# Optimization experiments

Hardware: AMD Instinct MI355X
Metric: run time of the kernel (lower is better)

The kernel has to match this reference:

```python
import jax, jax.numpy as jnp
import numpy as np
import math

B, SQ, SK, HID, NH = 2, 2048, 512, 1024, 16
HD = HID // NH  # head dim = 64


def setup_inputs() -> dict:
    key = jax.random.key(0)
    k1, k2, k3, k4, k5 = jax.random.split(key, 5)
    return {
        "hidden_states": jax.random.normal(k1, (B, SQ, HID), dtype=jnp.float32),
        "encoder_hidden_states": jax.random.normal(k2, (B, SK, HID), dtype=jnp.float32),
        "encoder_attention_mask": jnp.ones((B, SK), dtype=jnp.int32),
        "Wq": jax.random.normal(k3, (HID, HID), dtype=jnp.float32) * (1.0 / math.sqrt(HID)),
        "Wk": jax.random.normal(k4, (HID, HID), dtype=jnp.float32) * (1.0 / math.sqrt(HID)),
        "Wv": jax.random.normal(k5, (HID, HID), dtype=jnp.float32) * (1.0 / math.sqrt(HID)),
    }


def reference(hidden_states, encoder_hidden_states, encoder_attention_mask, Wq, Wk, Wv):
    # nn.Linear(bias=False): y = x @ W.T ; split heads -> [B, H, S, D]
    def split_heads(x, S):
        return x.reshape(x.shape[0], S, NH, HD).transpose(0, 2, 1, 3)

    q = split_heads(hidden_states @ Wq.T, SQ)            # [B,H,Sq,D]
    k = split_heads(encoder_hidden_states @ Wk.T, SK)    # [B,H,Sk,D]
    v = split_heads(encoder_hidden_states @ Wv.T, SK)    # [B,H,Sk,D]

    scores = jnp.einsum("bhqd,bhkd->bhqk", q, k) / math.sqrt(HD)  # [B,H,Sq,Sk]

    # HF-style extended mask: (1 - mask) * finfo.min, broadcast over heads/queries
    neg = jnp.finfo(scores.dtype).min
    inv_mask = (1.0 - encoder_attention_mask.astype(scores.dtype))[:, None, None, :] * neg

    probs = jax.nn.softmax(scores + inv_mask, axis=-1)
    context = jnp.einsum("bhqk,bhkd->bhqd", probs, v)    # [B,H,Sq,D]
    context = context.transpose(0, 2, 1, 3).reshape(hidden_states.shape[0], SQ, HID)
    # NOTE: returned attention_scores are scaled but UNMASKED, matching the source
    return (context, scores)
```

## Files before the change

kernel.cpp:

```cpp
#include <hip/hip_runtime.h>

#define B_   2
#define SQ_  2048
#define SK_  512
#define HID_ 1024
#define NH_  16
#define HD_  64

typedef __bf16 bf16x8 __attribute__((ext_vector_type(8)));
typedef float  f32x4  __attribute__((ext_vector_type(4)));

__device__ __forceinline__ unsigned short f2bf(float f) {
    unsigned u = __builtin_bit_cast(unsigned, f);
    u += 0x7fffu + ((u >> 16) & 1u);
    return (unsigned short)(u >> 16);
}

__device__ __forceinline__ void gll16(const unsigned short* g, unsigned short* l) {
    __builtin_amdgcn_global_load_lds(
        (const __attribute__((address_space(1))) unsigned int*)(const void*)g,
        (__attribute__((address_space(3))) unsigned int*)(void*)l,
        16, 0, 0);
}

__global__ __launch_bounds__(256) void cvt_all(const float* __restrict__ hs,
                                               const float* __restrict__ enc,
                                               const float* __restrict__ wq,
                                               const float* __restrict__ wk,
                                               const float* __restrict__ wv,
                                               unsigned short* __restrict__ hb,
                                               unsigned short* __restrict__ eb,
                                               unsigned short* __restrict__ wqb,
                                               unsigned short* __restrict__ wkb,
                                               unsigned short* __restrict__ wvb) {
    size_t i = ((size_t)blockIdx.x * 256 + threadIdx.x) * 4;
    const float* s; unsigned short* d; size_t off;
    if (i < 4194304)      { s = hs;  d = hb;  off = i; }
    else if (i < 5242880) { s = enc; d = eb;  off = i - 4194304; }
    else if (i < 6291456) { s = wq;  d = wqb; off = i - 5242880; }
    else if (i < 7340032) { s = wk;  d = wkb; off = i - 6291456; }
    else                  { s = wv;  d = wvb; off = i - 7340032; }
    float4 v = *reinterpret_cast<const float4*>(s + off);
    ushort4 o;
    o.x = f2bf(v.x); o.y = f2bf(v.y); o.z = f2bf(v.z); o.w = f2bf(v.w);
    *reinterpret_cast<ushort4*>(d + off) = o;
}

__global__ __launch_bounds__(256, 3) void gemm_qkv(const unsigned short* __restrict__ hb,
                                                   const unsigned short* __restrict__ eb,
                                                   const unsigned short* __restrict__ wq,
                                                   const unsigned short* __restrict__ wk,
                                                   const unsigned short* __restrict__ wv,
                                                   unsigned short* __restrict__ qo,
                                                   unsigned short* __restrict__ ko,
                                                   unsigned short* __restrict__ vo) {
    __shared__ unsigned short as[2][64 * 64];
    __shared__ unsigned short bs[2][128 * 64];

    int bid = blockIdx.x;
    bid = (bid & 7) * 96 + (bid >> 3);
    int nb = bid & 7, ms = bid >> 3;
    const unsigned short* Ab; const unsigned short* Wb;
    int mrow, mode;
    if (ms < 64)      { mode = 0; Ab = hb; Wb = wq; mrow = ms * 64; }
    else if (ms < 80) { mode = 1; Ab = eb; Wb = wk; mrow = (ms - 64) * 64; }
    else              { mode = 2; Ab = eb; Wb = wv; mrow = (ms - 80) * 64; }
    int n0 = nb * 128;

    int tid = threadIdx.x, lane = tid & 63, w = tid >> 6;
    int quad = lane >> 4, lc = lane & 15;

    int lr  = lane >> 3;
    int chg = (lane & 7) ^ lr;

    f32x4 zero4 = {0.f, 0.f, 0.f, 0.f};
    f32x4 acc[4][2];
#pragma unroll
    for (int i = 0; i < 4; i++) { acc[i][0] = zero4; acc[i][1] = zero4; }

    int rsw = lc & 7;

#pragma unroll
    for (int j = 0; j < 2; j++) {
        int c = w * 2 + j;
        gll16(Ab + (size_t)(mrow + c * 8 + lr) * 1024 + chg * 8, &as[0][(c * 8) * 64]);
    }
#pragma unroll
    for (int j = 0; j < 4; j++) {
        int c = w * 4 + j;
        gll16(Wb + (size_t)(n0 + c * 8 + lr) * 1024 + chg * 8, &bs[0][(c * 8) * 64]);
    }
    __syncthreads();

#pragma unroll 2
    for (int it = 0; it < 16; ++it) {
        int cur = it & 1;
        if (it < 15) {
            int k0n = (it + 1) * 64;
#pragma unroll
            for (int j = 0; j < 2; j++) {
                int c = w * 2 + j;
                gll16(Ab + (size_t)(mrow + c * 8 + lr) * 1024 + k0n + chg * 8,
                      &as[cur ^ 1][(c * 8) * 64]);
            }
#pragma unroll
            for (int j = 0; j < 4; j++) {
                int c = w * 4 + j;
                gll16(Wb + (size_t)(n0 + c * 8 + lr) * 1024 + k0n + chg * 8,
                      &bs[cur ^ 1][(c * 8) * 64]);
            }
        }
#pragma unroll
        for (int kk = 0; kk < 2; kk++) {
            bf16x8 af[4], bfr[2];
#pragma unroll
            for (int mt = 0; mt < 4; mt++)
                af[mt] = *reinterpret_cast<const bf16x8*>(
                    &as[cur][(mt * 16 + lc) * 64 + ((kk * 4 + quad) ^ rsw) * 8]);
#pragma unroll
            for (int nt = 0; nt < 2; nt++)
                bfr[nt] = *reinterpret_cast<const bf16x8*>(
                    &bs[cur][(w * 32 + nt * 16 + lc) * 64 + ((kk * 4 + quad) ^ rsw) * 8]);
#pragma unroll
            for (int mt = 0; mt < 4; mt++)
#pragma unroll
                for (int nt = 0; nt < 2; nt++)
                    acc[mt][nt] = __builtin_amdgcn_mfma_f32_16x16x32_bf16(af[mt], bfr[nt], acc[mt][nt], 0, 0, 0);
        }
        __syncthreads();
    }

#pragma unroll
    for (int mt = 0; mt < 4; mt++) {
#pragma unroll
        for (int nt = 0; nt < 2; nt++) {
            int n = n0 + w * 32 + nt * 16 + lc;
            int h = n >> 6, d = n & 63;
#pragma unroll
            for (int r = 0; r < 4; r++) {
                int M = mrow + mt * 16 + quad * 4 + r;
                unsigned short val = f2bf(acc[mt][nt][r]);
                if (mode == 0) {
                    int b = M >> 11, s = M & 2047;
                    qo[(((size_t)(b * NH_ + h)) * SQ_ + s) * HD_ + d] = val;
                } else if (mode == 1) {
                    int b = M >> 9, s = M & 511;
                    ko[(((size_t)(b * NH_ + h)) * SK_ + s) * HD_ + d] = val;
                } else {
                    int b = M >> 9, s = M & 511;
                    vo[(((size_t)(b * NH_ + h)) * HD_ + d) * SK_ + s] = val;
                }
            }
        }
    }
}

#define PST 72

__global__ __launch_bounds__(256, 4) void attn_kernel(const unsigned short* __restrict__ qh,
                                                      const unsigned short* __restrict__ kh,
                                                      const unsigned short* __restrict__ vh,
                                                      const int* __restrict__ maskp,
                                                      float* __restrict__ octx,
                                                      float* __restrict__ oscores) {
    __shared__ unsigned short qs[64 * 64];
    __shared__ unsigned short ks[64 * 64];
    __shared__ unsigned short vts[64 * 64];
    __shared__ unsigned short ps[64 * PST];
    __shared__ float lm[SK_];

    int bid = blockIdx.x;
    bid = (bid & 7) * 128 + (bid >> 3);
    int qt = bid & 31;
    int h  = (bid >> 5) & 15;
    int b  = bid >> 9;

    int tid = threadIdx.x, lane = tid & 63, w = tid >> 6;
    int quad = lane >> 4, lc = lane & 15;
    int wrow = w * 16;

    const unsigned short* qp = qh + ((size_t)(b * NH_ + h) * SQ_ + qt * 64) * HD_;
    const unsigned short* kp = kh + ((size_t)(b * NH_ + h) * SK_) * HD_;
    const unsigned short* vp = vh + ((size_t)(b * NH_ + h) * HD_) * SK_;

    int lr  = lane >> 3;
    int chg = (lane & 7) ^ lr;

#pragma unroll
    for (int j = 0; j < 2; j++) {
        int c = w * 2 + j;
        gll16(qp + (c * 8 + lr) * 64 + chg * 8, &qs[c * 512]);
        gll16(kp + (c * 8 + lr) * 64 + chg * 8, &ks[c * 512]);
        gll16(vp + (size_t)(c * 8 + lr) * SK_ + chg * 8, &vts[c * 512]);
    }
#pragma unroll
    for (int i = 0; i < 2; i++) {
        int c = tid + i * 256;
        lm[c] = maskp[b * SK_ + c] ? -23.0831227f : -3.0e38f;
    }
    __syncthreads();

    int rsw = lc & 7;
    bf16x8 qf[2];
#pragma unroll
    for (int hf = 0; hf < 2; hf++)
        qf[hf] = *reinterpret_cast<const bf16x8*>(&qs[(wrow + lc) * 64 + ((quad + hf * 4) ^ rsw) * 8]);
    __syncthreads();

    f32x4 zero4 = {0.f, 0.f, 0.f, 0.f};
    f32x4 cacc[4];
#pragma unroll
    for (int ct = 0; ct < 4; ct++) cacc[ct] = zero4;
    float lsum = 0.0f;

    float* srowp = oscores + ((size_t)(b * NH_ + h) * SQ_ + qt * 64 + wrow + lc) * SK_;

    for (int kt = 0; kt < 8; kt++) {
        const unsigned short* kcur = (kt & 1) ? qs : ks;
        if (kt < 7) {
            unsigned short* knxt = (kt & 1) ? ks : qs;
#pragma unroll
            for (int j = 0; j < 2; j++) {
                int c = w * 2 + j;
                gll16(kp + ((kt + 1) * 64 + c * 8 + lr) * 64 + chg * 8, &knxt[c * 512]);
            }
        }

        f32x4 s[4];
#pragma unroll
        for (int tl = 0; tl < 4; tl++) s[tl] = zero4;
        __builtin_amdgcn_s_setprio(1);
#pragma unroll
        for (int tl = 0; tl < 4; tl++) {
#pragma unroll
            for (int hf = 0; hf < 2; hf++) {
                bf16x8 kf = *reinterpret_cast<const bf16x8*>(
                    &kcur[(tl * 16 + lc) * 64 + ((quad + hf * 4) ^ rsw) * 8]);
                s[tl] = __builtin_amdgcn_mfma_f32_16x16x32_bf16(kf, qf[hf], s[tl], 0, 0, 0);
            }
        }
        __builtin_amdgcn_s_setprio(0);

#pragma unroll
        for (int tl = 0; tl < 4; tl++) {
            f32x4 sc = s[tl] * 0.125f;
            *reinterpret_cast<f32x4*>(&srowp[(kt * 4 + tl) * 16 + quad * 4]) = sc;
        }

#pragma unroll
        for (int tl = 0; tl < 4; tl++) {
            float4 mv = *reinterpret_cast<const float4*>(&lm[(kt * 4 + tl) * 16 + quad * 4]);
            float e0 = __builtin_amdgcn_exp2f(fmaf(s[tl][0], 0.1803369f, mv.x));
            float e1 = __builtin_amdgcn_exp2f(fmaf(s[tl][1], 0.1803369f, mv.y));
            float e2 = __builtin_amdgcn_exp2f(fmaf(s[tl][2], 0.1803369f, mv.z));
            float e3 = __builtin_amdgcn_exp2f(fmaf(s[tl][3], 0.1803369f, mv.w));
            lsum += (e0 + e1) + (e2 + e3);
            unsigned plo, phi;
            asm("v_cvt_pk_bf16_f32 %0, %1, %2" : "=v"(plo) : "v"(e0), "v"(e1));
            asm("v_cvt_pk_bf16_f32 %0, %1, %2" : "=v"(phi) : "v"(e2), "v"(e3));
            uint2 pk; pk.x = plo; pk.y = phi;
            *reinterpret_cast<uint2*>(&ps[(wrow + lc) * PST + tl * 16 + quad * 4]) = pk;
        }

        __builtin_amdgcn_s_setprio(1);
#pragma unroll
        for (int ks2 = 0; ks2 < 2; ks2++) {
            bf16x8 af = *reinterpret_cast<const bf16x8*>(&ps[(wrow + lc) * PST + ks2 * 32 + quad * 8]);
#pragma unroll
            for (int ct = 0; ct < 4; ct++) {
                bf16x8 bv = *reinterpret_cast<const bf16x8*>(
                    &vts[(ct * 16 + lc) * 64 + ((quad + ks2 * 4) ^ rsw) * 8]);
                cacc[ct] = __builtin_amdgcn_mfma_f32_16x16x32_bf16(af, bv, cacc[ct], 0, 0, 0);
            }
        }
        __builtin_amdgcn_s_setprio(0);

        __syncthreads();
        if (kt < 7) {
#pragma unroll
            for (int j = 0; j < 2; j++) {
                int c = w * 2 + j;
                gll16(vp + (size_t)(c * 8 + lr) * SK_ + (kt + 1) * 64 + chg * 8, &vts[c * 512]);
            }
            __syncthreads();
        }
    }

    lsum += __shfl_xor(lsum, 16);
    lsum += __shfl_xor(lsum, 32);
    float linv[4];
#pragma unroll
    for (int r = 0; r < 4; r++) linv[r] = 1.0f / __shfl(lsum, quad * 4 + r);
#pragma unroll
    for (int ct = 0; ct < 4; ct++) {
        int d = ct * 16 + lc;
#pragma unroll
        for (int r = 0; r < 4; r++) {
            int s = qt * 64 + wrow + quad * 4 + r;
            octx[((size_t)b * SQ_ + s) * HID_ + h * HD_ + d] = cacc[ct][r] * linv[r];
        }
    }
}

extern "C" void kernel_launch(void* const* d_in, const int* in_sizes, int n_in,
                              void* d_out, int out_size, void* d_ws, size_t ws_size,
                              hipStream_t stream) {
    const float* hs   = (const float*)d_in[0];
    const float* enc  = (const float*)d_in[1];
    const int*   mask = (const int*)d_in[2];
    const float* Wq   = (const float*)d_in[3];
    const float* Wk   = (const float*)d_in[4];
    const float* Wv   = (const float*)d_in[5];
    float* out = (float*)d_out;

    unsigned short* hb  = (unsigned short*)d_ws;
    unsigned short* eb  = hb  + 4194304;
    unsigned short* wqb = eb  + 1048576;
    unsigned short* wkb = wqb + 1048576;
    unsigned short* wvb = wkb + 1048576;
    unsigned short* qhp = wvb + 1048576;
    unsigned short* khp = qhp + 4194304;
    unsigned short* vhp = khp + 1048576;

    cvt_all<<<8192, 256, 0, stream>>>(hs, enc, Wq, Wk, Wv, hb, eb, wqb, wkb, wvb);
    gemm_qkv<<<768, 256, 0, stream>>>(hb, eb, wqb, wkb, wvb, qhp, khp, vhp);
    attn_kernel<<<1024, 256, 0, stream>>>(qhp, khp, vhp, mask, out, out + 4194304);
}
```

Measured before the change: 212.0 us.

## Double-buffer V tiles and overlap their prefetch with K in attention loop

V tiles now live in a two-slot LDS buffer. Each V tile is prefetched at the start of the iteration together with the next K tile, instead of being loaded after the PV MFMAs behind two block barriers. The per-iteration sync becomes a vmcnt wait plus a single s_barrier, which removes one barrier and the exposed V load latency. The probability staging buffer is halved and the exp/convert work is interleaved with the PV MFMAs per 32-column half. The cost is more LDS for the second V buffer and reliance on a hand-set vmcnt count that assumes the score stores are the only newer memory operations.

Measured after the change: 212.5 us. No clear change (+0.3%).

```diff
diff --git a/kernel.cpp b/kernel.cpp
--- a/kernel.cpp
+++ b/kernel.cpp
@@ -155,7 +155,7 @@
     }
 }
 
-#define PST 72
+#define PSH 36
 
 __global__ __launch_bounds__(256, 4) void attn_kernel(const unsigned short* __restrict__ qh,
                                                       const unsigned short* __restrict__ kh,
@@ -165,8 +165,8 @@
                                                       float* __restrict__ oscores) {
     __shared__ unsigned short qs[64 * 64];
     __shared__ unsigned short ks[64 * 64];
-    __shared__ unsigned short vts[64 * 64];
-    __shared__ unsigned short ps[64 * PST];
+    __shared__ unsigned short vts[2][64 * 64];
+    __shared__ unsigned short ps[64 * PSH];
     __shared__ float lm[SK_];
 
     int bid = blockIdx.x;
@@ -191,7 +191,7 @@
         int c = w * 2 + j;
         gll16(qp + (c * 8 + lr) * 64 + chg * 8, &qs[c * 512]);
         gll16(kp + (c * 8 + lr) * 64 + chg * 8, &ks[c * 512]);
-        gll16(vp + (size_t)(c * 8 + lr) * SK_ + chg * 8, &vts[c * 512]);
+        gll16(vp + (size_t)(c * 8 + lr) * SK_ + chg * 8, &vts[0][c * 512]);
     }
 #pragma unroll
     for (int i = 0; i < 2; i++) {
@@ -217,13 +217,18 @@
 
     for (int kt = 0; kt < 8; kt++) {
         const unsigned short* kcur = (kt & 1) ? qs : ks;
+        const unsigned short* vcur = vts[kt & 1];
+
         if (kt < 7) {
             unsigned short* knxt = (kt & 1) ? ks : qs;
+            unsigned short* vnxt = vts[(kt + 1) & 1];
 #pragma unroll
             for (int j = 0; j < 2; j++) {
                 int c = w * 2 + j;
                 gll16(kp + ((kt + 1) * 64 + c * 8 + lr) * 64 + chg * 8, &knxt[c * 512]);
-            }
+                gll16(vp + (size_t)(c * 8 + lr) * SK_ + (kt + 1) * 64 + chg * 8, &vnxt[c * 512]);
+            }
+            __builtin_amdgcn_sched_barrier(0);
         }
 
         f32x4 s[4];
@@ -248,41 +253,37 @@
         }
 
 #pragma unroll
-        for (int tl = 0; tl < 4; tl++) {
-            float4 mv = *reinterpret_cast<const float4*>(&lm[(kt * 4 + tl) * 16 + quad * 4]);
-            float e0 = __builtin_amdgcn_exp2f(fmaf(s[tl][0], 0.1803369f, mv.x));
-            float e1 = __builtin_amdgcn_exp2f(fmaf(s[tl][1], 0.1803369f, mv.y));
-            float e2 = __builtin_amdgcn_exp2f(fmaf(s[tl][2], 0.1803369f, mv.z));
-            float e3 = __builtin_amdgcn_exp2f(fmaf(s[tl][3], 0.1803369f, mv.w));
-            lsum += (e0 + e1) + (e2 + e3);
-            unsigned plo, phi;
-            asm("v_cvt_pk_bf16_f32 %0, %1, %2" : "=v"(plo) : "v"(e0), "v"(e1));
-            asm("v_cvt_pk_bf16_f32 %0, %1, %2" : "=v"(phi) : "v"(e2), "v"(e3));
-            uint2 pk; pk.x = plo; pk.y = phi;
-            *reinterpret_cast<uint2*>(&ps[(wrow + lc) * PST + tl * 16 + quad * 4]) = pk;
-        }
-
-        __builtin_amdgcn_s_setprio(1);
-#pragma unroll
         for (int ks2 = 0; ks2 < 2; ks2++) {
-            bf16x8 af = *reinterpret_cast<const bf16x8*>(&ps[(wrow + lc) * PST + ks2 * 32 + quad * 8]);
+#pragma unroll
+            for (int u = 0; u < 2; u++) {
+                int t = ks2 * 2 + u;
+                float4 mv = *reinterpret_cast<const float4*>(&lm[(kt * 4 + t) * 16 + quad * 4]);
+                float e0 = __builtin_amdgcn_exp2f(fmaf(s[t][0], 0.1803369f, mv.x));
+                float e1 = __builtin_amdgcn_exp2f(fmaf(s[t][1], 0.1803369f, mv.y));
+                float e2 = __builtin_amdgcn_exp2f(fmaf(s[t][2], 0.1803369f, mv.z));
+                float e3 = __builtin_amdgcn_exp2f(fmaf(s[t][3], 0.1803369f, mv.w));
+                lsum += (e0 + e1) + (e2 + e3);
+                unsigned plo, phi;
+                asm("v_cvt_pk_bf16_f32 %0, %1, %2" : "=v"(plo) : "v"(e0), "v"(e1));
+                asm("v_cvt_pk_bf16_f32 %0, %1, %2" : "=v"(phi) : "v"(e2), "v"(e3));
+                uint2 pk; pk.x = plo; pk.y = phi;
+                *reinterpret_cast<uint2*>(&ps[(wrow + lc) * PSH + u * 16 + quad * 4]) = pk;
+            }
+            bf16x8 af = *reinterpret_cast<const bf16x8*>(&ps[(wrow + lc) * PSH + quad * 8]);
+            __builtin_amdgcn_s_setprio(1);
 #pragma unroll
             for (int ct = 0; ct < 4; ct++) {
                 bf16x8 bv = *reinterpret_cast<const bf16x8*>(
-                    &vts[(ct * 16 + lc) * 64 + ((quad + ks2 * 4) ^ rsw) * 8]);
+                    &vcur[(ct * 16 + lc) * 64 + ((quad + ks2 * 4) ^ rsw) * 8]);
                 cacc[ct] = __builtin_amdgcn_mfma_f32_16x16x32_bf16(af, bv, cacc[ct], 0, 0, 0);
             }
-        }
-        __builtin_amdgcn_s_setprio(0);
-
-        __syncthreads();
+            __builtin_amdgcn_s_setprio(0);
+        }
+
         if (kt < 7) {
-#pragma unroll
-            for (int j = 0; j < 2; j++) {
-                int c = w * 2 + j;
-                gll16(vp + (size_t)(c * 8 + lr) * SK_ + (kt + 1) * 64 + chg * 8, &vts[c * 512]);
-            }
-            __syncthreads();
+            asm volatile("s_waitcnt vmcnt(4)" ::: "memory");
+            __builtin_amdgcn_s_barrier();
+            __builtin_amdgcn_sched_barrier(0);
         }
     }
 
```
